# Performance work log

Hardware: AMD Instinct MI355X
Metric: run time of the kernel (lower is better)

Reference implementation:

```python
import jax, jax.numpy as jnp
import numpy as np

NUM_NODES = 262144        # 1024 graphs x 256 nodes
NODES_PER_GRAPH = 256
NUM_GRAPHS = NUM_NODES // NODES_PER_GRAPH
NUM_EDGES = 2097152       # avg degree 8
NUM_FEATURES = 9
NUM_STATIONS = 8


def setup_inputs() -> dict:
    key = jax.random.key(0)
    ks = jax.random.split(key, 12)
    # edges constrained within each graph so batched-graph semantics hold
    src_local = jax.random.randint(ks[0], (NUM_EDGES,), 0, NODES_PER_GRAPH)
    dst_local = jax.random.randint(ks[1], (NUM_EDGES,), 0, NODES_PER_GRAPH)
    graph_of_edge = jax.random.randint(ks[2], (NUM_EDGES,), 0, NUM_GRAPHS)
    offset = graph_of_edge * NODES_PER_GRAPH
    edge_index = jnp.stack([src_local + offset, dst_local + offset]).astype(jnp.int64)
    station_ids = jnp.array([0, 37, 73, 110, 146, 183, 219, 255], dtype=jnp.int64)
    s = lambda k, shape, fan_in: jax.random.normal(k, shape, jnp.float32) / np.sqrt(fan_in)
    return {
        "x": jax.random.normal(ks[3], (NUM_NODES, NUM_FEATURES), jnp.float32),
        "edge_index": edge_index,
        "station_ids": station_ids,
        "W1": s(ks[4], (NUM_FEATURES, 32), NUM_FEATURES),
        "b1": jnp.zeros((32,), jnp.float32),
        "W2": s(ks[5], (32, 64), 32),
        "b2": jnp.zeros((64,), jnp.float32),
        "fc1_W": s(ks[6], (128, 64), 128),
        "fc1_b": jnp.zeros((64,), jnp.float32),
        "fc2_W": s(ks[7], (64, 1), 64),
        "fc2_b": jnp.zeros((1,), jnp.float32),
    }


def _gcn_conv(x, W, b, src, dst, n_nodes):
    """PyG GCNConv: add self-loops, symmetric normalization, linear first."""
    h = x @ W                                              # [N, C_out]
    # degree includes the self-loop (+1), counted on target nodes
    deg = jnp.zeros((n_nodes,), h.dtype).at[dst].add(1.0) + 1.0
    dinv = jax.lax.rsqrt(deg)                              # deg >= 1, safe
    norm = dinv[src] * dinv[dst]                           # [E]
    out = jnp.zeros_like(h).at[dst].add(norm[:, None] * h[src])
    out = out + (dinv * dinv)[:, None] * h                 # self-loop term
    return out + b


def reference(x, edge_index, station_ids, W1, b1, W2, b2, fc1_W, fc1_b, fc2_W, fc2_b):
    n = x.shape[0]
    src, dst = edge_index[0], edge_index[1]
    h = jax.nn.relu(_gcn_conv(x, W1, b1, src, dst, n))     # [N, 32]
    h = jax.nn.relu(_gcn_conv(h, W2, b2, src, dst, n))     # [N, 64]
    # global mean pool per graph (batch = node_idx // NODES_PER_GRAPH)
    batch = jnp.arange(n) // NODES_PER_GRAPH
    sums = jax.ops.segment_sum(h, batch, num_segments=NUM_GRAPHS)
    counts = jax.ops.segment_sum(jnp.ones((n,), h.dtype), batch, num_segments=NUM_GRAPHS)
    global_ctx = sums / counts[:, None]                    # [B, 64]
    # per-station gather-MLP, vectorized over stations
    idx = jnp.arange(NUM_GRAPHS)[:, None] * NODES_PER_GRAPH + station_ids[None, :]  # [B, S]
    station_emb = h[idx]                                   # [B, S, 64]
    ctx = jnp.broadcast_to(global_ctx[:, None, :], station_emb.shape)
    combined = jnp.concatenate([station_emb, ctx], axis=-1)  # [B, S, 128]
    q = jax.nn.relu(combined @ fc1_W + fc1_b) @ fc2_W + fc2_b  # [B, S, 1]
    return q[..., 0]                                       # [B, S]
```

## Files before the change

kernel.cpp:

```cpp
#include <hip/hip_runtime.h>
#include <hip/hip_bf16.h>


#define NNODES 262144
#define NPG 256
#define NGRAPHS 1024
#define NEDGES 2097152
#define NFEAT 9
#define ECAP2 2560
#define T_EDGES 8192
#define NTILES (NEDGES / T_EDGES)
#define TPB 1024
#define NBLK 256

typedef __hip_bfloat16 bf16;
typedef short short8 __attribute__((ext_vector_type(8)));
typedef float f32x4 __attribute__((ext_vector_type(4)));

__device__ __forceinline__ float bfbits(unsigned short u) { return __uint_as_float(((unsigned)u) << 16); }
__device__ __forceinline__ unsigned short f2bbits(float v) { bf16 b = __float2bfloat16(v); return *(unsigned short*)&b; }


__global__ void __launch_bounds__(1024) k_hist(const int* __restrict__ dst,
                                               int* __restrict__ hist) {
    __shared__ int cnt[NGRAPHS];
    int t = threadIdx.x;
    cnt[t] = 0;
    __syncthreads();
    const int4* d4 = (const int4*)(dst + blockIdx.x * T_EDGES);
#pragma unroll
    for (int k = 0; k < T_EDGES / 4096; ++k) {
        int4 dv = d4[k * 1024 + t];
        atomicAdd(&cnt[dv.x >> 8], 1);
        atomicAdd(&cnt[dv.y >> 8], 1);
        atomicAdd(&cnt[dv.z >> 8], 1);
        atomicAdd(&cnt[dv.w >> 8], 1);
    }
    __syncthreads();
    hist[blockIdx.x * NGRAPHS + t] = cnt[t];
}

__global__ void __launch_bounds__(256) k_scan(int* __restrict__ hist,
                                              int* __restrict__ gcnt) {
    __shared__ int wsum[4];
    int g = blockIdx.x;
    int t = threadIdx.x;
    int lane = t & 63, wv = t >> 6;
    int v = hist[t * NGRAPHS + g];
    int inc = v;
    for (int off = 1; off < 64; off <<= 1) {
        int y = __shfl_up(inc, off);
        if (lane >= off) inc += y;
    }
    if (lane == 63) wsum[wv] = inc;
    __syncthreads();
    int wpre = 0;
#pragma unroll
    for (int w = 0; w < 3; ++w) if (w < wv) wpre += wsum[w];
    int exc = wpre + inc - v;
    hist[t * NGRAPHS + g] = exc;
    if (t == 255) gcnt[g * 16] = exc + v;
}

__global__ void __launch_bounds__(1024) k_scatter(const int* __restrict__ src,
                                                  const int* __restrict__ dst,
                                                  const int* __restrict__ hist,
                                                  unsigned short* __restrict__ gout) {
    __shared__ unsigned short sg[T_EDGES];
    __shared__ unsigned short pay[T_EDGES];
    __shared__ unsigned short spay[T_EDGES];
    __shared__ unsigned short ssg[T_EDGES];
    __shared__ int cnt[NGRAPHS];
    __shared__ int lbase[NGRAPHS];
    __shared__ int gb[NGRAPHS];
    __shared__ int wsum[16];
    int t = threadIdx.x;
    int lane = t & 63, wv = t >> 6;
    int base = blockIdx.x * T_EDGES;
    cnt[t] = 0;
    gb[t] = hist[blockIdx.x * NGRAPHS + t];
    __syncthreads();
    const int4* s4 = (const int4*)(src + base);
    const int4* d4 = (const int4*)(dst + base);
#pragma unroll
    for (int k = 0; k < T_EDGES / 4096; ++k) {
        int idx = k * 1024 + t;
        int4 dv = d4[idx];
        int4 sv = s4[idx];
        int i0 = idx * 4;
        sg[i0]     = (unsigned short)(dv.x >> 8);
        sg[i0 + 1] = (unsigned short)(dv.y >> 8);
        sg[i0 + 2] = (unsigned short)(dv.z >> 8);
        sg[i0 + 3] = (unsigned short)(dv.w >> 8);
        pay[i0]     = (unsigned short)(((dv.x & 255) << 8) | (sv.x & 255));
        pay[i0 + 1] = (unsigned short)(((dv.y & 255) << 8) | (sv.y & 255));
        pay[i0 + 2] = (unsigned short)(((dv.z & 255) << 8) | (sv.z & 255));
        pay[i0 + 3] = (unsigned short)(((dv.w & 255) << 8) | (sv.w & 255));
        atomicAdd(&cnt[dv.x >> 8], 1);
        atomicAdd(&cnt[dv.y >> 8], 1);
        atomicAdd(&cnt[dv.z >> 8], 1);
        atomicAdd(&cnt[dv.w >> 8], 1);
    }
    __syncthreads();
    int c = cnt[t];
    int inc = c;
    for (int off = 1; off < 64; off <<= 1) {
        int y = __shfl_up(inc, off);
        if (lane >= off) inc += y;
    }
    if (lane == 63) wsum[wv] = inc;
    __syncthreads();
    int wpre = 0;
    for (int w = 0; w < wv; ++w) wpre += wsum[w];
    lbase[t] = wpre + inc - c;
    cnt[t] = 0;
    __syncthreads();
#pragma unroll
    for (int k = 0; k < T_EDGES / 1024; ++k) {
        int i = k * 1024 + t;
        int g = sg[i];
        int p = lbase[g] + atomicAdd(&cnt[g], 1);
        spay[p] = pay[i];
        ssg[p] = (unsigned short)g;
    }
    __syncthreads();
#pragma unroll
    for (int k = 0; k < T_EDGES / 1024; ++k) {
        int p = k * 1024 + t;
        int g = ssg[p];
        int off = gb[g] + (p - lbase[g]);
        if (off < ECAP2) gout[(size_t)g * ECAP2 + off] = spay[p];
    }
}


__global__ void __launch_bounds__(TPB) k_fused(
    const float* __restrict__ x, const int* __restrict__ station_ids,
    const float* __restrict__ W1, const float* __restrict__ b1,
    const float* __restrict__ W2, const float* __restrict__ b2,
    const float* __restrict__ fc1W, const float* __restrict__ fc1b,
    const float* __restrict__ fc2W, const float* __restrict__ fc2b,
    const int* __restrict__ gcnt, const unsigned short* __restrict__ gedges,
    float* __restrict__ out) {

    __shared__ __align__(16) unsigned char Ms[131072];
    __shared__ __align__(16) unsigned char Buf[16384];
    __shared__ __align__(16) unsigned short EPa[ECAP2];
    __shared__ unsigned char El[ECAP2];
    __shared__ unsigned int sru[256];
    __shared__ unsigned short Rl[260];
    __shared__ float dinvs[256];
    __shared__ float W1s[288];
    __shared__ float sts[512];
    __shared__ float poolf[64];
    __shared__ float spart[8];
    __shared__ unsigned char stmap[256];
    __shared__ float b1s[32], b2s[64], fc1bs[64], fc2ws[64];
    __shared__ int stids[8];
    __shared__ float fc2bv;

    int t = threadIdx.x;
    int lane = t & 63, wvid = t >> 6;
    int m = lane & 15, quad = lane >> 4;

    for (int i = t; i < NFEAT * 32; i += TPB) W1s[i] = W1[i];
    if (t < 32) b1s[t] = b1[t];
    if (t < 64) { b2s[t] = b2[t]; fc1bs[t] = fc1b[t]; fc2ws[t] = fc2W[t]; }
    if (t < 8) { stids[t] = station_ids[t]; spart[t] = 0.f; }
    if (t == 0) fc2bv = fc2b[0];
    if (t < 256) stmap[t] = 255;
    short8 w2f[4];
#pragma unroll
    for (int ni = 0; ni < 4; ++ni)
#pragma unroll
        for (int j = 0; j < 8; ++j)
            w2f[ni][j] = (short)f2bbits(W2[(quad * 8 + j) * 64 + ni * 16 + m]);
    short8 fc1f[4];
    {
        int ni = wvid & 3;
#pragma unroll
        for (int kt = 0; kt < 4; ++kt)
#pragma unroll
            for (int j = 0; j < 8; ++j)
                fc1f[kt][j] = (short)f2bbits(fc1W[((kt * 4 + quad) * 8 + j) * 64 + ni * 16 + m]);
    }
    __syncthreads();
    if (t < 8) stmap[stids[t] & 255] = (unsigned char)t;

    for (int g = blockIdx.x; g < NGRAPHS; g += NBLK) {

        int ecnt = min(gcnt[g * 16], ECAP2);
        {
            const uint4* gev = (const uint4*)(gedges + (size_t)g * ECAP2);
            uint4* epv = (uint4*)EPa;
            for (int i = t; i < ECAP2 / 8; i += TPB) epv[i] = gev[i];
        }
        if (t < 256) sru[t] = 0u;
        if (t >= 256 && t < 320) poolf[t - 256] = 0.f;
        __syncthreads();

        if (t < 8) spart[t] = 0.f;
        for (int i = t; i < ecnt; i += TPB) atomicAdd(&sru[EPa[i] >> 8], 1u);
        __syncthreads();

        if (wvid == 0) {
            int b0 = sru[lane * 4], b1v = sru[lane * 4 + 1];
            int b2v = sru[lane * 4 + 2], b3 = sru[lane * 4 + 3];
            int s = b0 + b1v + b2v + b3;
            int inc = s;
            for (int off = 1; off < 64; off <<= 1) {
                int y = __shfl_up(inc, off);
                if (lane >= off) inc += y;
            }
            int r0 = inc - s;
            int r1 = r0 + b0, r2 = r1 + b1v, r3 = r2 + b2v;
            Rl[lane * 4] = (unsigned short)r0;     dinvs[lane * 4] = rsqrtf((float)(b0 + 1));
            Rl[lane * 4 + 1] = (unsigned short)r1; dinvs[lane * 4 + 1] = rsqrtf((float)(b1v + 1));
            Rl[lane * 4 + 2] = (unsigned short)r2; dinvs[lane * 4 + 2] = rsqrtf((float)(b2v + 1));
            Rl[lane * 4 + 3] = (unsigned short)r3; dinvs[lane * 4 + 3] = rsqrtf((float)(b3 + 1));
            sru[lane * 4] = r0; sru[lane * 4 + 1] = r1;
            sru[lane * 4 + 2] = r2; sru[lane * 4 + 3] = r3;
            if (lane == 63) Rl[256] = (unsigned short)inc;
        }
        __syncthreads();

        for (int i = t; i < ecnt; i += TPB) {
            unsigned short v = EPa[i];
            unsigned p = atomicAdd(&sru[v >> 8], 1u);
            if (p < ECAP2) El[p] = (unsigned char)(v & 255);
        }
        __syncthreads();

        if (t < 512) {
            int d = t >> 1, q = t & 1;
            uint4* mz = (uint4*)(Ms + d * 512 + q * 256);
            uint4 z = {0u, 0u, 0u, 0u};
#pragma unroll
            for (int i = 0; i < 16; ++i) mz[i] = z;
            float did = dinvs[d];
            if ((d >> 7) == q)
                *(unsigned short*)(Ms + d * 512 + (((d >> 3) ^ (d & 15)) * 16) + (d & 7) * 2)
                    = f2bbits(did * did);
            int r0 = Rl[d], r1 = Rl[d + 1];
            for (int e = r0; e < r1; ++e) {
                int s = El[e];
                if ((s >> 7) == q) {
                    unsigned short* p =
                        (unsigned short*)(Ms + d * 512 + (((s >> 3) ^ (d & 15)) * 16) + (s & 7) * 2);
                    *p = f2bbits(bfbits(*p) + did * dinvs[s]);
                }
            }
        } else {
            int tt = t - 512;
            int n = tt >> 1, half = tt & 1;
            const float* xr = x + (size_t)(g * NPG + n) * NFEAT;
            float xv[NFEAT];
#pragma unroll
            for (int k = 0; k < NFEAT; ++k) xv[k] = xr[k];
            int c0 = half * 16;
#pragma unroll 4
            for (int ci = 0; ci < 16; ++ci) {
                int c = c0 + ci;
                float acc = 0.f;
#pragma unroll
                for (int k = 0; k < NFEAT; ++k) acc += xv[k] * W1s[k * 32 + c];
                *(unsigned short*)(Buf + c * 512 + (((n >> 3) ^ (c & 15)) * 16) + (n & 7) * 2)
                    = f2bbits(acc);
            }
        }
        __syncthreads();

        f32x4 acc1[2] = {};
        for (int kt = 0; kt < 8; ++kt) {
            short8 af = *(const short8*)(Ms + (size_t)(wvid * 16 + m) * 512 + (((kt * 4 + quad) ^ m) * 16));
            short8 bf0 = *(const short8*)(Buf + (size_t)m * 512 + (((kt * 4 + quad) ^ m) * 16));
            short8 bf1 = *(const short8*)(Buf + (size_t)(16 + m) * 512 + (((kt * 4 + quad) ^ m) * 16));
            acc1[0] = __builtin_amdgcn_mfma_f32_16x16x32_bf16(af, bf0, acc1[0], 0, 0, 0);
            acc1[1] = __builtin_amdgcn_mfma_f32_16x16x32_bf16(af, bf1, acc1[1], 0, 0, 0);
        }
        __syncthreads();

#pragma unroll
        for (int ct = 0; ct < 2; ++ct) {
            int ch = ct * 16 + m;
            float bb = b1s[ch];
#pragma unroll
            for (int r = 0; r < 4; ++r) {
                int node = wvid * 16 + quad * 4 + r;
                *(unsigned short*)(Buf + (size_t)ch * 512 + (((node >> 3) ^ (ch & 15)) * 16) + (node & 7) * 2)
                    = f2bbits(fmaxf(acc1[ct][r] + bb, 0.f));
            }
        }
        __syncthreads();

        {
            f32x4 a2[2] = {};
            for (int kt = 0; kt < 8; ++kt) {
                short8 af = *(const short8*)(Ms + (size_t)(wvid * 16 + m) * 512 + (((kt * 4 + quad) ^ m) * 16));
                short8 bf0 = *(const short8*)(Buf + (size_t)m * 512 + (((kt * 4 + quad) ^ m) * 16));
                short8 bf1 = *(const short8*)(Buf + (size_t)(16 + m) * 512 + (((kt * 4 + quad) ^ m) * 16));
                a2[0] = __builtin_amdgcn_mfma_f32_16x16x32_bf16(af, bf0, a2[0], 0, 0, 0);
                a2[1] = __builtin_amdgcn_mfma_f32_16x16x32_bf16(af, bf1, a2[1], 0, 0, 0);
            }
#pragma unroll
            for (int ct = 0; ct < 2; ++ct) {
                int ch = ct * 16 + m;
                int c8 = ch >> 3;
#pragma unroll
                for (int r = 0; r < 4; ++r) {
                    int node = wvid * 16 + quad * 4 + r;
                    *(unsigned short*)(Ms + (size_t)node * 512 + ((c8 ^ (node & 3)) * 16) + (ch & 7) * 2)
                        = f2bbits(a2[ct][r]);
                }
            }
        }
        __syncthreads();

        {
            int mt = wvid;
            short8 af = *(const short8*)(Ms + (size_t)(mt * 16 + m) * 512 + ((quad ^ (m & 3)) * 16));
#pragma unroll
            for (int ni = 0; ni < 4; ++ni) {
                f32x4 c = {};
                c = __builtin_amdgcn_mfma_f32_16x16x32_bf16(af, w2f[ni], c, 0, 0, 0);
                int ch = ni * 16 + m;
                float bb = b2s[ch];
                float hv[4];
                float p = 0.f;
#pragma unroll
                for (int r = 0; r < 4; ++r) { hv[r] = fmaxf(c[r] + bb, 0.f); p += hv[r]; }
                p += __shfl_down(p, 32);
                p += __shfl_down(p, 16);
                if (quad == 0) atomicAdd(&poolf[ch], p);
#pragma unroll
                for (int r = 0; r < 4; ++r) {
                    int node = mt * 16 + quad * 4 + r;
                    int si = stmap[node];
                    if (si != 255) sts[si * 64 + ch] = hv[r];
                }
            }
        }
        __syncthreads();

        if (wvid < 4) {
            short8 af4[4];
#pragma unroll
            for (int kt = 0; kt < 4; ++kt) {
#pragma unroll
                for (int j = 0; j < 8; ++j) {
                    int k = kt * 32 + quad * 8 + j;
                    float v = 0.f;
                    if (m < 8) v = (k < 64) ? sts[m * 64 + k] : poolf[k - 64] * (1.0f / 256.0f);
                    af4[kt][j] = (short)f2bbits(v);
                }
            }
            f32x4 c = {};
#pragma unroll
            for (int kt = 0; kt < 4; ++kt)
                c = __builtin_amdgcn_mfma_f32_16x16x32_bf16(af4[kt], fc1f[kt], c, 0, 0, 0);
            int ch = wvid * 16 + m;
            float fb = fc1bs[ch], fw = fc2ws[ch];
#pragma unroll
            for (int r = 0; r < 4; ++r) {
                float a = fmaxf(c[r] + fb, 0.f) * fw;
#pragma unroll
                for (int off = 1; off < 16; off <<= 1) a += __shfl_xor(a, off);
                int st = quad * 4 + r;
                if (m == 0 && st < 8) atomicAdd(&spart[st], a);
            }
        }
        __syncthreads();

        if (t < 8) out[g * 8 + t] = spart[t] + fc2bv;
    }
}


extern "C" void kernel_launch(void* const* d_in, const int* in_sizes, int n_in,
                              void* d_out, int out_size, void* d_ws, size_t ws_size,
                              hipStream_t stream) {
    const float* x = (const float*)d_in[0];
    const int* ei = (const int*)d_in[1];
    const int* station_ids = (const int*)d_in[2];
    const float* W1 = (const float*)d_in[3];
    const float* b1 = (const float*)d_in[4];
    const float* W2 = (const float*)d_in[5];
    const float* bias2 = (const float*)d_in[6];
    const float* fc1W = (const float*)d_in[7];
    const float* fc1b = (const float*)d_in[8];
    const float* fc2W = (const float*)d_in[9];
    const float* fc2b = (const float*)d_in[10];
    float* out = (float*)d_out;
    (void)in_sizes; (void)n_in; (void)out_size; (void)ws_size;

    char* ws = (char*)d_ws;
    int* gcnt = (int*)ws;
    unsigned short* gout = (unsigned short*)(ws + 0x10000);
    int* hist = (int*)(ws + 0x510000);

    const int* esrc = ei;
    const int* edst = ei + NEDGES;

    k_hist<<<NTILES, 1024, 0, stream>>>(edst, hist);
    k_scan<<<NGRAPHS, 256, 0, stream>>>(hist, gcnt);
    k_scatter<<<NTILES, 1024, 0, stream>>>(esrc, edst, hist, gout);
    k_fused<<<NBLK, TPB, 0, stream>>>(x, station_ids, W1, b1, W2, bias2,
                                      fc1W, fc1b, fc2W, fc2b, gcnt, gout, out);
}
```

Measured before the change: 166.5 us.

## Compute first-layer X@W1 with MFMA and split adjacency build across all threads

The first GCN linear transform moves from scalar FMAs on half the block to a bf16 MFMA per wave, with W1 held in register fragments (K padded from 9 to 32 with zeros). The per-graph adjacency matrix construction is now spread over all 1024 threads (4 per row) instead of 512, with a swizzled zeroing pattern. This removes the split where half the block built adjacency while the other half did slow scalar matmul. In exchange, x is rounded to bf16 before the first matmul, and each edge list is now scanned by four threads instead of two.

```diff
diff --git a/kernel.cpp b/kernel.cpp
--- a/kernel.cpp
+++ b/kernel.cpp
@@ -150,7 +150,6 @@
     __shared__ unsigned int sru[256];
     __shared__ unsigned short Rl[260];
     __shared__ float dinvs[256];
-    __shared__ float W1s[288];
     __shared__ float sts[512];
     __shared__ float poolf[64];
     __shared__ float spart[8];
@@ -163,7 +162,6 @@
     int lane = t & 63, wvid = t >> 6;
     int m = lane & 15, quad = lane >> 4;
 
-    for (int i = t; i < NFEAT * 32; i += TPB) W1s[i] = W1[i];
     if (t < 32) b1s[t] = b1[t];
     if (t < 64) { b2s[t] = b2[t]; fc1bs[t] = fc1b[t]; fc2ws[t] = fc2W[t]; }
     if (t < 8) { stids[t] = station_ids[t]; spart[t] = 0.f; }
@@ -184,6 +182,14 @@
             for (int j = 0; j < 8; ++j)
                 fc1f[kt][j] = (short)f2bbits(fc1W[((kt * 4 + quad) * 8 + j) * 64 + ni * 16 + m]);
     }
+    short8 w1f[2];
+#pragma unroll
+    for (int ct = 0; ct < 2; ++ct)
+#pragma unroll
+        for (int j = 0; j < 8; ++j) {
+            int k = quad * 8 + j;
+            w1f[ct][j] = (short)(k < NFEAT ? f2bbits(W1[k * 32 + ct * 16 + m]) : 0);
+        }
     __syncthreads();
     if (t < 8) stmap[stids[t] & 255] = (unsigned char)t;
 
@@ -231,41 +237,58 @@
         }
         __syncthreads();
 
-        if (t < 512) {
-            int d = t >> 1, q = t & 1;
-            uint4* mz = (uint4*)(Ms + d * 512 + q * 256);
+        {
+            int node = wvid * 16 + m;
+            const float* xr = x + (size_t)(g * NPG + node) * NFEAT;
+            float xv0 = 0.f, xv1 = 0.f, xv2 = 0.f, xv3 = 0.f;
+            float xv4 = 0.f, xv5 = 0.f, xv6 = 0.f, xv7 = 0.f;
+            if (quad == 0) {
+                xv0 = xr[0]; xv1 = xr[1]; xv2 = xr[2]; xv3 = xr[3];
+                xv4 = xr[4]; xv5 = xr[5]; xv6 = xr[6]; xv7 = xr[7];
+            } else if (quad == 1) {
+                xv0 = xr[8];
+            }
+
+            int d = t >> 2, q = t & 3;
+            int qz = q ^ ((d >> 3) & 1);
+            uint4* mz = (uint4*)(Ms + d * 512 + qz * 128);
             uint4 z = {0u, 0u, 0u, 0u};
 #pragma unroll
-            for (int i = 0; i < 16; ++i) mz[i] = z;
+            for (int i = 0; i < 8; ++i) mz[i] = z;
             float did = dinvs[d];
-            if ((d >> 7) == q)
+            if ((d >> 6) == q)
                 *(unsigned short*)(Ms + d * 512 + (((d >> 3) ^ (d & 15)) * 16) + (d & 7) * 2)
                     = f2bbits(did * did);
             int r0 = Rl[d], r1 = Rl[d + 1];
             for (int e = r0; e < r1; ++e) {
                 int s = El[e];
-                if ((s >> 7) == q) {
+                if ((s >> 6) == q) {
                     unsigned short* p =
                         (unsigned short*)(Ms + d * 512 + (((s >> 3) ^ (d & 15)) * 16) + (s & 7) * 2);
                     *p = f2bbits(bfbits(*p) + did * dinvs[s]);
                 }
             }
-        } else {
-            int tt = t - 512;
-            int n = tt >> 1, half = tt & 1;
-            const float* xr = x + (size_t)(g * NPG + n) * NFEAT;
-            float xv[NFEAT];
-#pragma unroll
-            for (int k = 0; k < NFEAT; ++k) xv[k] = xr[k];
-            int c0 = half * 16;
-#pragma unroll 4
-            for (int ci = 0; ci < 16; ++ci) {
-                int c = c0 + ci;
-                float acc = 0.f;
-#pragma unroll
-                for (int k = 0; k < NFEAT; ++k) acc += xv[k] * W1s[k * 32 + c];
-                *(unsigned short*)(Buf + c * 512 + (((n >> 3) ^ (c & 15)) * 16) + (n & 7) * 2)
-                    = f2bbits(acc);
+
+            short8 af = {};
+            if (quad == 0) {
+                af[0] = (short)f2bbits(xv0); af[1] = (short)f2bbits(xv1);
+                af[2] = (short)f2bbits(xv2); af[3] = (short)f2bbits(xv3);
+                af[4] = (short)f2bbits(xv4); af[5] = (short)f2bbits(xv5);
+                af[6] = (short)f2bbits(xv6); af[7] = (short)f2bbits(xv7);
+            } else if (quad == 1) {
+                af[0] = (short)f2bbits(xv0);
+            }
+#pragma unroll
+            for (int ct = 0; ct < 2; ++ct) {
+                f32x4 c = {};
+                c = __builtin_amdgcn_mfma_f32_16x16x32_bf16(af, w1f[ct], c, 0, 0, 0);
+                int ch = ct * 16 + m;
+#pragma unroll
+                for (int r = 0; r < 4; ++r) {
+                    int nn = wvid * 16 + quad * 4 + r;
+                    *(unsigned short*)(Buf + (size_t)ch * 512 + (((nn >> 3) ^ (ch & 15)) * 16) + (nn & 7) * 2)
+                        = f2bbits(c[r]);
+                }
             }
         }
         __syncthreads();
```

Result: slower. 175.5 us (+5.4%).

## Move per-graph edge CSR build into separate fully-parallel sort kernel

Applied to the files above, without the earlier changes.

Adds a k_sort2 kernel with one block per graph (1024 blocks). It counts edges per destination, scans, computes dinv, and writes a compact CSR blob (sorted src bytes, dinv, row offsets) to the workspace. The fused kernel, which runs only 256 blocks, now just loads this precomputed blob instead of doing the histogram, scan and scatter with several barriers per graph. Pool and spart resets move to the end of the loop. The cost is an extra kernel launch and a global-memory round trip for the blob.

```diff
diff --git a/kernel.cpp b/kernel.cpp
--- a/kernel.cpp
+++ b/kernel.cpp
@@ -12,6 +12,7 @@
 #define NTILES (NEDGES / T_EDGES)
 #define TPB 1024
 #define NBLK 256
+#define EBSTRIDE 4608
 
 typedef __hip_bfloat16 bf16;
 typedef short short8 __attribute__((ext_vector_type(8)));
@@ -133,6 +134,50 @@
     }
 }
 
+__global__ void __launch_bounds__(256) k_sort2(const int* __restrict__ gcnt,
+                                               const unsigned short* __restrict__ gout,
+                                               unsigned char* __restrict__ eblob) {
+    __shared__ unsigned short ep[ECAP2];
+    __shared__ unsigned int cnt[256];
+    __shared__ unsigned int base[256];
+    __shared__ int wsum[4];
+    int g = blockIdx.x;
+    int t = threadIdx.x;
+    int lane = t & 63, wv = t >> 6;
+    int ecnt = min(gcnt[g * 16], ECAP2);
+    cnt[t] = 0;
+    {
+        const uint4* gev = (const uint4*)(gout + (size_t)g * ECAP2);
+        uint4* epv = (uint4*)ep;
+        for (int i = t; i < ECAP2 / 8; i += 256) epv[i] = gev[i];
+    }
+    __syncthreads();
+    for (int i = t; i < ecnt; i += 256) atomicAdd(&cnt[ep[i] >> 8], 1u);
+    __syncthreads();
+    int c = (int)cnt[t];
+    int inc = c;
+    for (int off = 1; off < 64; off <<= 1) {
+        int y = __shfl_up(inc, off);
+        if (lane >= off) inc += y;
+    }
+    if (lane == 63) wsum[wv] = inc;
+    __syncthreads();
+    int wpre = 0;
+    for (int w = 0; w < wv; ++w) wpre += wsum[w];
+    int exc = wpre + inc - c;
+    unsigned char* eb = eblob + (size_t)g * EBSTRIDE;
+    ((unsigned short*)(eb + 3584))[t] = (unsigned short)exc;
+    if (t == 255) ((unsigned short*)(eb + 3584))[256] = (unsigned short)(exc + c);
+    ((float*)(eb + 2560))[t] = rsqrtf((float)(c + 1));
+    base[t] = (unsigned)exc;
+    __syncthreads();
+    for (int i = t; i < ecnt; i += 256) {
+        unsigned short v = ep[i];
+        unsigned p = atomicAdd(&base[v >> 8], 1u);
+        if (p < ECAP2) eb[p] = (unsigned char)(v & 255);
+    }
+}
+
 
 __global__ void __launch_bounds__(TPB) k_fused(
     const float* __restrict__ x, const int* __restrict__ station_ids,
@@ -140,16 +185,13 @@
     const float* __restrict__ W2, const float* __restrict__ b2,
     const float* __restrict__ fc1W, const float* __restrict__ fc1b,
     const float* __restrict__ fc2W, const float* __restrict__ fc2b,
-    const int* __restrict__ gcnt, const unsigned short* __restrict__ gedges,
-    float* __restrict__ out) {
+    const unsigned char* __restrict__ eblob, float* __restrict__ out) {
 
     __shared__ __align__(16) unsigned char Ms[131072];
     __shared__ __align__(16) unsigned char Buf[16384];
-    __shared__ __align__(16) unsigned short EPa[ECAP2];
-    __shared__ unsigned char El[ECAP2];
-    __shared__ unsigned int sru[256];
-    __shared__ unsigned short Rl[260];
-    __shared__ float dinvs[256];
+    __shared__ __align__(16) unsigned char El[ECAP2];
+    __shared__ __align__(16) float dinvs[256];
+    __shared__ __align__(4) unsigned short Rl[260];
     __shared__ float W1s[288];
     __shared__ float sts[512];
     __shared__ float poolf[64];
@@ -165,7 +207,7 @@
 
     for (int i = t; i < NFEAT * 32; i += TPB) W1s[i] = W1[i];
     if (t < 32) b1s[t] = b1[t];
-    if (t < 64) { b2s[t] = b2[t]; fc1bs[t] = fc1b[t]; fc2ws[t] = fc2W[t]; }
+    if (t < 64) { b2s[t] = b2[t]; fc1bs[t] = fc1b[t]; fc2ws[t] = fc2W[t]; poolf[t] = 0.f; }
     if (t < 8) { stids[t] = station_ids[t]; spart[t] = 0.f; }
     if (t == 0) fc2bv = fc2b[0];
     if (t < 256) stmap[t] = 255;
@@ -189,45 +231,14 @@
 
     for (int g = blockIdx.x; g < NGRAPHS; g += NBLK) {
 
-        int ecnt = min(gcnt[g * 16], ECAP2);
         {
-            const uint4* gev = (const uint4*)(gedges + (size_t)g * ECAP2);
-            uint4* epv = (uint4*)EPa;
-            for (int i = t; i < ECAP2 / 8; i += TPB) epv[i] = gev[i];
-        }
-        if (t < 256) sru[t] = 0u;
-        if (t >= 256 && t < 320) poolf[t - 256] = 0.f;
-        __syncthreads();
-
-        if (t < 8) spart[t] = 0.f;
-        for (int i = t; i < ecnt; i += TPB) atomicAdd(&sru[EPa[i] >> 8], 1u);
-        __syncthreads();
-
-        if (wvid == 0) {
-            int b0 = sru[lane * 4], b1v = sru[lane * 4 + 1];
-            int b2v = sru[lane * 4 + 2], b3 = sru[lane * 4 + 3];
-            int s = b0 + b1v + b2v + b3;
-            int inc = s;
-            for (int off = 1; off < 64; off <<= 1) {
-                int y = __shfl_up(inc, off);
-                if (lane >= off) inc += y;
-            }
-            int r0 = inc - s;
-            int r1 = r0 + b0, r2 = r1 + b1v, r3 = r2 + b2v;
-            Rl[lane * 4] = (unsigned short)r0;     dinvs[lane * 4] = rsqrtf((float)(b0 + 1));
-            Rl[lane * 4 + 1] = (unsigned short)r1; dinvs[lane * 4 + 1] = rsqrtf((float)(b1v + 1));
-            Rl[lane * 4 + 2] = (unsigned short)r2; dinvs[lane * 4 + 2] = rsqrtf((float)(b2v + 1));
-            Rl[lane * 4 + 3] = (unsigned short)r3; dinvs[lane * 4 + 3] = rsqrtf((float)(b3 + 1));
-            sru[lane * 4] = r0; sru[lane * 4 + 1] = r1;
-            sru[lane * 4 + 2] = r2; sru[lane * 4 + 3] = r3;
-            if (lane == 63) Rl[256] = (unsigned short)inc;
-        }
-        __syncthreads();
-
-        for (int i = t; i < ecnt; i += TPB) {
-            unsigned short v = EPa[i];
-            unsigned p = atomicAdd(&sru[v >> 8], 1u);
-            if (p < ECAP2) El[p] = (unsigned char)(v & 255);
+            const unsigned char* eb = eblob + (size_t)g * EBSTRIDE;
+            const uint4* ev = (const uint4*)eb;
+            const uint4* dv = (const uint4*)(eb + 2560);
+            const unsigned int* rv = (const unsigned int*)(eb + 3584);
+            for (int i = t; i < 160; i += TPB) ((uint4*)El)[i] = ev[i];
+            for (int i = t; i < 64; i += TPB) ((uint4*)dinvs)[i] = dv[i];
+            for (int i = t; i < 129; i += TPB) ((unsigned int*)Rl)[i] = rv[i];
         }
         __syncthreads();
 
@@ -371,7 +382,8 @@
         }
         __syncthreads();
 
-        if (t < 8) out[g * 8 + t] = spart[t] + fc2bv;
+        if (t < 8) { out[g * 8 + t] = spart[t] + fc2bv; spart[t] = 0.f; }
+        if (t >= 64 && t < 128) poolf[t - 64] = 0.f;
     }
 }
 
@@ -397,6 +409,7 @@
     int* gcnt = (int*)ws;
     unsigned short* gout = (unsigned short*)(ws + 0x10000);
     int* hist = (int*)(ws + 0x510000);
+    unsigned char* eblob = (unsigned char*)(ws + 0x610000);
 
     const int* esrc = ei;
     const int* edst = ei + NEDGES;
@@ -404,6 +417,7 @@
     k_hist<<<NTILES, 1024, 0, stream>>>(edst, hist);
     k_scan<<<NGRAPHS, 256, 0, stream>>>(hist, gcnt);
     k_scatter<<<NTILES, 1024, 0, stream>>>(esrc, edst, hist, gout);
+    k_sort2<<<NGRAPHS, 256, 0, stream>>>(gcnt, gout, eblob);
     k_fused<<<NBLK, TPB, 0, stream>>>(x, station_ids, W1, b1, W2, bias2,
-                                      fc1W, fc1b, fc2W, fc2b, gcnt, gout, out);
-}
+                                      fc1W, fc1b, fc2W, fc2b, eblob, out);
+}
```

After: 167.7 us. About the same (+0.7%).
